# Optimization experiments

Measured on AMD Instinct MI355X. Metric: run time of the kernel, lower is better.

## Reference

```python
import jax, jax.numpy as jnp
import numpy as np
from jax import lax

T, B, D = 2048, 16, 1024

def _xavier(key, shape):
    limit = np.sqrt(6.0 / (shape[0] + shape[1])).astype(np.float32)
    return jax.random.uniform(key, shape, jnp.float32, -limit, limit)

def setup_inputs() -> dict:
    key = jax.random.key(0)
    kx, ka, kk, kv = jax.random.split(key, 4)
    return {
        "x": jax.random.normal(kx, (T, B, D), jnp.float32),
        "h0": jnp.zeros((B, D), jnp.float32),
        "W_alpha": _xavier(ka, (D, D)),
        "b_alpha": jnp.full((D,), 2.0, jnp.float32),
        "W_k": _xavier(kk, (D, D)),
        "b_k": jnp.full((D,), -2.0, jnp.float32),
        "W_v": _xavier(kv, (D, D)),
        "b_v": jnp.zeros((D,), jnp.float32),
    }

def reference(x, h0, W_alpha, b_alpha, W_k, b_k, W_v, b_v):
    # Gate projections: x @ W.T + b, batched over (T, B). Shapes: [T,B,D]
    alpha = jax.nn.sigmoid(jnp.einsum('tbd,ed->tbe', x, W_alpha) + b_alpha)
    k = jax.nn.sigmoid(jnp.einsum('tbd,ed->tbe', x, W_k) + b_k)
    v = jnp.tanh(jnp.einsum('tbd,ed->tbe', x, W_v) + b_v)
    retain = alpha * (1.0 - k)   # a_t
    write = k * v                # b_t
    # Diagonal linear recurrence h_t = a_t * h_{t-1} + b_t via scan
    def step(h, ab):
        a, b = ab
        h_new = a * h + b
        return h_new, h_new
    _, hs = lax.scan(step, h0, (retain, write))  # hs: [T,B,D]
    h = jnp.concatenate([h0[None], hs], axis=0)  # [T+1,B,D], includes h0
    # output_t = h_t * silu(h_t) = h_t^2 * sigmoid(h_t)
    output = hs * hs * jax.nn.sigmoid(hs)
    return (output, h)
```

## Files before the change

### kernel.cpp

```cpp
#include <hip/hip_runtime.h>
#include <cstdint>

#define T_DIM 2048
#define B_DIM 16
#define D_DIM 1024
#define M_DIM (T_DIM * B_DIM)
#define BD (B_DIM * D_DIM)
#define BD4 (BD / 4)
#define CCH 64
#define LCH (T_DIM / CCH)

typedef _Float16 f16x8 __attribute__((ext_vector_type(8)));
typedef float f32x4 __attribute__((ext_vector_type(4)));

__device__ __forceinline__ void async_cp16(const void* g, void* l) {
  __builtin_amdgcn_global_load_lds(
      (const __attribute__((address_space(1))) void*)(uintptr_t)g,
      (__attribute__((address_space(3))) void*)(uint32_t)(uintptr_t)l,
      16, 0, 0);
}

__device__ __forceinline__ float sigmoidf_(float z) {
  return 1.f / (1.f + __expf(-z));
}
__device__ __forceinline__ float tanhf_(float z) {
  float t = __expf(2.f * z);
  return (t - 1.f) / (t + 1.f);
}

__global__ void cvt_f32_f16(const float* __restrict__ s, _Float16* __restrict__ d, int n8) {
  int i = blockIdx.x * blockDim.x + threadIdx.x;
  if (i >= n8) return;
  const float4* sp = (const float4*)s;
  float4 u = sp[2 * i];
  float4 v = sp[2 * i + 1];
  f16x8 o;
  o[0] = (_Float16)u.x; o[1] = (_Float16)u.y; o[2] = (_Float16)u.z; o[3] = (_Float16)u.w;
  o[4] = (_Float16)v.x; o[5] = (_Float16)v.y; o[6] = (_Float16)v.z; o[7] = (_Float16)v.w;
  *(f16x8*)(d + (size_t)i * 8) = o;
}

__global__ __launch_bounds__(512, 2) void gate_gemm(
    const _Float16* __restrict__ x16,
    const _Float16* __restrict__ wa16,
    const _Float16* __restrict__ wk16,
    const _Float16* __restrict__ wv16,
    const float* __restrict__ ba, const float* __restrict__ bk, const float* __restrict__ bv,
    float* __restrict__ Aret, float* __restrict__ Bwr) {
  __shared__ __align__(16) char smem[65536];
  auto sA = (_Float16 (*)[128][32])(smem);
  auto sB = (_Float16 (*)[3][128][32])(smem + 16384);

  const int tid  = threadIdx.x;
  const int wid  = tid >> 6;
  const int lane = tid & 63;
  const int wm = wid >> 2;
  const int wn = wid & 3;
  const int lr = lane & 15;
  const int kg = lane >> 4;

  const int m0 = blockIdx.x * 128;
  const int n0 = blockIdx.y * 128;

  const int arow = tid >> 2;
  const int achk = tid & 3;
  const int aswz = achk ^ ((arow >> 1) & 3);

  f32x4 acc[3][4][2];
#pragma unroll
  for (int w = 0; w < 3; ++w)
#pragma unroll
    for (int mi = 0; mi < 4; ++mi)
#pragma unroll
      for (int ni = 0; ni < 2; ++ni)
        acc[w][mi][ni] = (f32x4)0.f;

  const size_t gA0 = (size_t)(m0 + arow) * D_DIM + aswz * 8;
  const size_t gB0 = (size_t)(n0 + arow) * D_DIM + aswz * 8;

  auto stage = [&](int buf, int kk) {
    async_cp16(x16  + gA0 + kk * 32, (char*)&sA[buf][0][0]    + tid * 16);
    async_cp16(wa16 + gB0 + kk * 32, (char*)&sB[buf][0][0][0] + tid * 16);
    async_cp16(wk16 + gB0 + kk * 32, (char*)&sB[buf][1][0][0] + tid * 16);
    async_cp16(wv16 + gB0 + kk * 32, (char*)&sB[buf][2][0][0] + tid * 16);
  };

  const int slot = (kg ^ ((lr >> 1) & 3)) * 8;

  auto compute = [&](int buf) {
    f16x8 af[4];
#pragma unroll
    for (int mi = 0; mi < 4; ++mi)
      af[mi] = *(const f16x8*)&sA[buf][wm * 64 + mi * 16 + lr][slot];
#pragma unroll
    for (int w = 0; w < 3; ++w) {
      f16x8 b0 = *(const f16x8*)&sB[buf][w][wn * 32 + lr][slot];
      f16x8 b1 = *(const f16x8*)&sB[buf][w][wn * 32 + 16 + lr][slot];
#pragma unroll
      for (int mi = 0; mi < 4; ++mi) {
        acc[w][mi][0] = __builtin_amdgcn_mfma_f32_16x16x32_f16(af[mi], b0, acc[w][mi][0], 0, 0, 0);
        acc[w][mi][1] = __builtin_amdgcn_mfma_f32_16x16x32_f16(af[mi], b1, acc[w][mi][1], 0, 0, 0);
      }
    }
  };

  stage(0, 0);
  __syncthreads();
  int cur = 0;
#pragma unroll 1
  for (int kk = 0; kk < 32; ++kk) {
    if (kk + 1 < 32) stage(cur ^ 1, kk + 1);
    compute(cur);
    __syncthreads();
    cur ^= 1;
  }

  float* tb = (float*)smem + wid * (32 * 33);
  const float ba_[2] = { ba[n0 + wn * 32 + lr], ba[n0 + wn * 32 + 16 + lr] };
  const float bk_[2] = { bk[n0 + wn * 32 + lr], bk[n0 + wn * 32 + 16 + lr] };
  const float bv_[2] = { bv[n0 + wn * 32 + lr], bv[n0 + wn * 32 + 16 + lr] };

#pragma unroll
  for (int arr = 0; arr < 2; ++arr) {
    float* dst = arr ? Bwr : Aret;
#pragma unroll
    for (int half = 0; half < 2; ++half) {
#pragma unroll
      for (int ni = 0; ni < 2; ++ni)
#pragma unroll
        for (int m2 = 0; m2 < 2; ++m2) {
          const int mi = half * 2 + m2;
#pragma unroll
          for (int r = 0; r < 4; ++r) {
            float za = acc[0][mi][ni][r] + ba_[ni];
            float zk = acc[1][mi][ni][r] + bk_[ni];
            float val;
            if (arr == 0) {
              val = sigmoidf_(za) * (1.f - sigmoidf_(zk));
            } else {
              float zv = acc[2][mi][ni][r] + bv_[ni];
              val = sigmoidf_(zk) * tanhf_(zv);
            }
            tb[(m2 * 16 + kg * 4 + r) * 33 + ni * 16 + lr] = val;
          }
        }
      __syncthreads();
#pragma unroll
      for (int i = 0; i < 4; ++i) {
        const int rl = i * 8 + (lane >> 3);
        const int cc = (lane & 7) * 4;
        float4 v;
        v.x = tb[rl * 33 + cc + 0];
        v.y = tb[rl * 33 + cc + 1];
        v.z = tb[rl * 33 + cc + 2];
        v.w = tb[rl * 33 + cc + 3];
        const size_t m = (size_t)(m0 + wm * 64 + half * 32 + rl);
        *(float4*)&dst[m * D_DIM + n0 + wn * 32 + cc] = v;
      }
      __syncthreads();
    }
  }
}

__device__ __forceinline__ float4 f4fma(float4 a, float4 h, float4 b) {
  float4 r;
  r.x = fmaf(a.x, h.x, b.x); r.y = fmaf(a.y, h.y, b.y);
  r.z = fmaf(a.z, h.z, b.z); r.w = fmaf(a.w, h.w, b.w);
  return r;
}
__device__ __forceinline__ float4 f4mul(float4 a, float4 b) {
  float4 r; r.x = a.x*b.x; r.y = a.y*b.y; r.z = a.z*b.z; r.w = a.w*b.w; return r;
}

__global__ void scan_phase1(const float4* __restrict__ A4, const float4* __restrict__ B4,
                            float4* __restrict__ cP, float4* __restrict__ cS) {
  int tid = blockIdx.x * 256 + threadIdx.x;
  int bd4 = tid & (BD4 - 1);
  int c   = tid >> 12;
  size_t base = (size_t)c * LCH * BD4 + bd4;
  float4 P = make_float4(1.f, 1.f, 1.f, 1.f);
  float4 S = make_float4(0.f, 0.f, 0.f, 0.f);
#pragma unroll 4
  for (int t = 0; t < LCH; ++t) {
    float4 a = A4[base + (size_t)t * BD4];
    float4 b = B4[base + (size_t)t * BD4];
    S = f4fma(a, S, b);
    P = f4mul(P, a);
  }
  cP[tid] = P;
  cS[tid] = S;
}

__global__ void scan_phase2(const float4* __restrict__ h0q,
                            const float4* __restrict__ cP, const float4* __restrict__ cS,
                            float4* __restrict__ hst, float4* __restrict__ houtq) {
  int bd4 = blockIdx.x * 64 + threadIdx.x;
  float4 h = h0q[bd4];
  houtq[bd4] = h;
#pragma unroll 4
  for (int c = 0; c < CCH; ++c) {
    hst[(size_t)c * BD4 + bd4] = h;
    h = f4fma(cP[(size_t)c * BD4 + bd4], h, cS[(size_t)c * BD4 + bd4]);
  }
}

__global__ void scan_phase3(const float4* __restrict__ hst,
                            float4* __restrict__ Aq, float4* __restrict__ Bq) {
  int tid = blockIdx.x * 256 + threadIdx.x;
  int bd4 = tid & (BD4 - 1);
  int c   = tid >> 12;
  size_t base = (size_t)c * LCH * BD4 + bd4;
  float4 h = hst[(size_t)c * BD4 + bd4];
#pragma unroll 4
  for (int t = 0; t < LCH; ++t) {
    size_t off = base + (size_t)t * BD4;
    float4 a = Aq[off];
    float4 b = Bq[off];
    h = f4fma(a, h, b);
    Bq[off] = h;
    float4 o;
    o.x = h.x * h.x * sigmoidf_(h.x);
    o.y = h.y * h.y * sigmoidf_(h.y);
    o.z = h.z * h.z * sigmoidf_(h.z);
    o.w = h.w * h.w * sigmoidf_(h.w);
    Aq[off] = o;
  }
}

extern "C" void kernel_launch(void* const* d_in, const int* in_sizes, int n_in,
                              void* d_out, int out_size, void* d_ws, size_t ws_size,
                              hipStream_t stream) {
  const float* x  = (const float*)d_in[0];
  const float* h0 = (const float*)d_in[1];
  const float* Wa = (const float*)d_in[2];
  const float* ba = (const float*)d_in[3];
  const float* Wk = (const float*)d_in[4];
  const float* bk = (const float*)d_in[5];
  const float* Wv = (const float*)d_in[6];
  const float* bv = (const float*)d_in[7];

  float* out  = (float*)d_out;
  float* hout = out + (size_t)M_DIM * D_DIM;

  float* Aret = out;
  float* Bwr  = hout + BD;

  char* ws = (char*)d_ws;
  _Float16* x16  = (_Float16*)ws;
  _Float16* wa16 = (_Float16*)(ws + 67108864);
  _Float16* wk16 = (_Float16*)(ws + 67108864 + 2097152);
  _Float16* wv16 = (_Float16*)(ws + 67108864 + 2 * 2097152);
  float4* cP  = (float4*)ws;
  float4* cS  = cP + (size_t)CCH * BD4;
  float4* hst = cS + (size_t)CCH * BD4;

  const int nx8 = M_DIM * D_DIM / 8;
  const int nw8 = D_DIM * D_DIM / 8;
  cvt_f32_f16<<<dim3((nx8 + 255) / 256), dim3(256), 0, stream>>>(x, x16, nx8);
  cvt_f32_f16<<<dim3((nw8 + 255) / 256), dim3(256), 0, stream>>>(Wa, wa16, nw8);
  cvt_f32_f16<<<dim3((nw8 + 255) / 256), dim3(256), 0, stream>>>(Wk, wk16, nw8);
  cvt_f32_f16<<<dim3((nw8 + 255) / 256), dim3(256), 0, stream>>>(Wv, wv16, nw8);

  gate_gemm<<<dim3(M_DIM / 128, D_DIM / 128), dim3(512), 0, stream>>>(
      x16, wa16, wk16, wv16, ba, bk, bv, Aret, Bwr);

  scan_phase1<<<dim3(CCH * BD4 / 256), dim3(256), 0, stream>>>(
      (const float4*)Aret, (const float4*)Bwr, cP, cS);
  scan_phase2<<<dim3(BD4 / 64), dim3(64), 0, stream>>>(
      (const float4*)h0, cP, cS, hst, (float4*)hout);
  scan_phase3<<<dim3(CCH * BD4 / 256), dim3(256), 0, stream>>>(
      hst, (float4*)Aret, (float4*)Bwr);
}
```

Measured before the change: 784.1 us.

## Triple-buffer gate GEMM loads with explicit vmcnt waits and raw barriers

Moves the gate GEMM's K loop from double to triple buffering in LDS (96KB). Loads are issued two stages ahead, and explicit s_waitcnt vmcnt counts plus raw s_barrier replace __syncthreads. The goal is to hide global-to-LDS latency behind MFMA compute. The larger LDS footprint may cut the two-blocks-per-CU occupancy set by launch bounds, and the hand-written waitcnt counts depend on the exact number of loads issued per stage.

```diff
diff --git a/kernel.cpp b/kernel.cpp
--- a/kernel.cpp
+++ b/kernel.cpp
@@ -47,9 +47,7 @@
     const _Float16* __restrict__ wv16,
     const float* __restrict__ ba, const float* __restrict__ bk, const float* __restrict__ bv,
     float* __restrict__ Aret, float* __restrict__ Bwr) {
-  __shared__ __align__(16) char smem[65536];
-  auto sA = (_Float16 (*)[128][32])(smem);
-  auto sB = (_Float16 (*)[3][128][32])(smem + 16384);
+  __shared__ __align__(16) char smem[98304];
 
   const int tid  = threadIdx.x;
   const int wid  = tid >> 6;
@@ -79,23 +77,26 @@
   const size_t gB0 = (size_t)(n0 + arow) * D_DIM + aswz * 8;
 
   auto stage = [&](int buf, int kk) {
-    async_cp16(x16  + gA0 + kk * 32, (char*)&sA[buf][0][0]    + tid * 16);
-    async_cp16(wa16 + gB0 + kk * 32, (char*)&sB[buf][0][0][0] + tid * 16);
-    async_cp16(wk16 + gB0 + kk * 32, (char*)&sB[buf][1][0][0] + tid * 16);
-    async_cp16(wv16 + gB0 + kk * 32, (char*)&sB[buf][2][0][0] + tid * 16);
+    char* base = smem + buf * 32768;
+    async_cp16(x16  + gA0 + kk * 32, base         + tid * 16);
+    async_cp16(wa16 + gB0 + kk * 32, base +  8192 + tid * 16);
+    async_cp16(wk16 + gB0 + kk * 32, base + 16384 + tid * 16);
+    async_cp16(wv16 + gB0 + kk * 32, base + 24576 + tid * 16);
   };
 
   const int slot = (kg ^ ((lr >> 1) & 3)) * 8;
 
   auto compute = [&](int buf) {
+    const _Float16* bufA = (const _Float16*)(smem + buf * 32768);
+    const _Float16* bufB = bufA + 4096;
     f16x8 af[4];
 #pragma unroll
     for (int mi = 0; mi < 4; ++mi)
-      af[mi] = *(const f16x8*)&sA[buf][wm * 64 + mi * 16 + lr][slot];
+      af[mi] = *(const f16x8*)&bufA[(wm * 64 + mi * 16 + lr) * 32 + slot];
 #pragma unroll
     for (int w = 0; w < 3; ++w) {
-      f16x8 b0 = *(const f16x8*)&sB[buf][w][wn * 32 + lr][slot];
-      f16x8 b1 = *(const f16x8*)&sB[buf][w][wn * 32 + 16 + lr][slot];
+      f16x8 b0 = *(const f16x8*)&bufB[(w * 128 + wn * 32 + lr) * 32 + slot];
+      f16x8 b1 = *(const f16x8*)&bufB[(w * 128 + wn * 32 + 16 + lr) * 32 + slot];
 #pragma unroll
       for (int mi = 0; mi < 4; ++mi) {
         acc[w][mi][0] = __builtin_amdgcn_mfma_f32_16x16x32_f16(af[mi], b0, acc[w][mi][0], 0, 0, 0);
@@ -105,15 +106,26 @@
   };
 
   stage(0, 0);
-  __syncthreads();
-  int cur = 0;
+  stage(1, 1);
 #pragma unroll 1
-  for (int kk = 0; kk < 32; ++kk) {
-    if (kk + 1 < 32) stage(cur ^ 1, kk + 1);
-    compute(cur);
-    __syncthreads();
-    cur ^= 1;
-  }
+  for (int kk = 0; kk < 30; ++kk) {
+    stage((kk + 2) % 3, kk + 2);
+    asm volatile("s_waitcnt vmcnt(8)" ::: "memory");
+    __builtin_amdgcn_s_barrier();
+    compute(kk % 3);
+    asm volatile("s_waitcnt lgkmcnt(0)" ::: "memory");
+    __builtin_amdgcn_s_barrier();
+  }
+  asm volatile("s_waitcnt vmcnt(4)" ::: "memory");
+  __builtin_amdgcn_s_barrier();
+  compute(0);
+  asm volatile("s_waitcnt lgkmcnt(0)" ::: "memory");
+  __builtin_amdgcn_s_barrier();
+  asm volatile("s_waitcnt vmcnt(0)" ::: "memory");
+  __builtin_amdgcn_s_barrier();
+  compute(1);
+  asm volatile("s_waitcnt lgkmcnt(0)" ::: "memory");
+  __builtin_amdgcn_s_barrier();
 
   float* tb = (float*)smem + wid * (32 * 33);
   const float ba_[2] = { ba[n0 + wn * 32 + lr], ba[n0 + wn * 32 + 16 + lr] };
```

Result: faster. 764.6 us (-2.5%).
